# Optimization experiments

Hardware: AMD Instinct MI355X
Metric: run time of the kernel (lower is better)

Reference implementation:

```python
import jax, jax.numpy as jnp
import numpy as np

B, T, K, D, H, HL, S, KN = 4096, 50, 32, 64, 256, 128, 100000, 1000


def setup_inputs() -> dict:
    key = jax.random.key(0)
    ks = jax.random.split(key, 24)
    inp = {
        "uididx": jax.random.randint(ks[0], (B,), 0, S, dtype=jnp.int32),
        "kcodeidx": jax.random.randint(ks[1], (B, K), 0, KN, dtype=jnp.int32),
        "kcode_len": jax.random.randint(ks[2], (B,), 1, K + 1, dtype=jnp.int32),
        "qidemb": jax.random.normal(ks[3], (B, T, D), dtype=jnp.float32),
        "qid_len": jax.random.randint(ks[4], (B,), 1, T + 1, dtype=jnp.int32),
        # embedding tables
        "stuE": jax.random.normal(ks[5], (S, D), dtype=jnp.float32) * 0.1,
        "knE": jax.random.normal(ks[6], (KN, D), dtype=jnp.float32) * 0.1,
        # Theta DNN params
        "T_W1": jax.random.normal(ks[7], (D, H), dtype=jnp.float32) * (1.0 / np.sqrt(D)),
        "T_b1": jnp.zeros((H,), jnp.float32),
        "T_W2": jax.random.normal(ks[8], (H, 1), dtype=jnp.float32) * (1.0 / np.sqrt(H)),
        "T_b2": jnp.zeros((1,), jnp.float32),
        # A DNN params
        "A_W1": jax.random.normal(ks[9], (D, H), dtype=jnp.float32) * (1.0 / np.sqrt(D)),
        "A_b1": jnp.zeros((H,), jnp.float32),
        "A_W2": jax.random.normal(ks[10], (H, 1), dtype=jnp.float32) * (1.0 / np.sqrt(H)),
        "A_b2": jnp.zeros((1,), jnp.float32),
        # LSTM params (gate order i,f,g,o) + output head
        "L_Wi": jax.random.normal(ks[11], (D, 4 * HL), dtype=jnp.float32) * (1.0 / np.sqrt(D)),
        "L_Wh": jax.random.normal(ks[12], (HL, 4 * HL), dtype=jnp.float32) * (1.0 / np.sqrt(HL)),
        "L_b": jnp.zeros((4 * HL,), jnp.float32),
        "L_Wo": jax.random.normal(ks[13], (HL, 1), dtype=jnp.float32) * (1.0 / np.sqrt(HL)),
        "L_bo": jnp.zeros((1,), jnp.float32),
    }
    return inp


def _dnn(x, W1, b1, W2, b2):
    return jnp.tanh(x @ W1 + b1) @ W2 + b2


def _lstm_last(x, lengths, Wi, Wh, b):
    # x: [B,T,D]; returns last valid hidden state [B,HL]
    xg = jnp.einsum('btd,dh->bth', x, Wi) + b  # precomputed input projections
    h0 = jnp.zeros((x.shape[0], Wh.shape[0]), x.dtype)

    def step(carry, inp):
        h, c = carry
        g_x, t = inp
        g = g_x + h @ Wh
        i, f, gg, o = jnp.split(g, 4, axis=-1)
        c2 = jax.nn.sigmoid(f) * c + jax.nn.sigmoid(i) * jnp.tanh(gg)
        h2 = jax.nn.sigmoid(o) * jnp.tanh(c2)
        upd = (t < lengths)[:, None]
        return (jnp.where(upd, h2, h), jnp.where(upd, c2, c)), None

    (h, _), _ = jax.lax.scan(step, (h0, h0), (xg.transpose(1, 0, 2), jnp.arange(x.shape[1])))
    return h


def reference(uididx, kcodeidx, kcode_len, qidemb, qid_len, stuE, knE,
              T_W1, T_b1, T_W2, T_b2, A_W1, A_b1, A_W2, A_b2,
              L_Wi, L_Wh, L_b, L_Wo, L_bo):
    stu = stuE[uididx]            # [B,D]
    kemb = knE[kcodeidx]          # [B,K,D]
    kmask = jnp.arange(kcodeidx.shape[1])[None, :] < kcode_len[:, None]  # [B,K]
    kmf = kmask.astype(kemb.dtype)

    # per-student mastery: sigmoid(kemb @ stu / 5), then masked reductions
    mastery = jax.nn.sigmoid(jnp.einsum('bkd,bd->bk', kemb, stu) / 5.0)
    mastvec = jnp.einsum('bk,bkd->bd', mastery * kmf, kemb)  # sum(mastery * kemb)
    avec = jnp.einsum('bk,bkd->bd', kmf, kemb)               # sum(kemb)

    # scaled dot-product attention: q=qidemb, k=v=kemb, scale=0.15
    scores = jnp.einsum('btd,bkd->btk', qidemb, kemb) * 0.15
    scores = jnp.where(kmask[:, None, :], scores, -1e9)
    attw = jax.nn.softmax(scores, axis=-1)
    bvec = jnp.einsum('btk,bkd->btd', attw, kemb)            # [B,T,D]

    t = _dnn(mastvec, T_W1, T_b1, T_W2, T_b2)                             # theta [B,1]
    a = 8.0 * (jax.nn.sigmoid(jnp.abs(_dnn(avec, A_W1, A_b1, A_W2, A_b2))) - 0.5)
    hT = _lstm_last(bvec, qid_len, L_Wi, L_Wh, L_b)
    b = 8.0 * (jax.nn.sigmoid(hT @ L_Wo + L_bo) - 0.5)                    # [B,1]

    return jax.nn.sigmoid(a * (t - b))  # IRT response probability [B,1]
```

## Files before the change

kernel.cpp:

```cpp
#include <hip/hip_runtime.h>
#include <math.h>

#define B_  4096
#define T_  50
#define K_  32
#define D_  64
#define H_  256
#define HL_ 128
#define G4_ 512

typedef __attribute__((ext_vector_type(8))) short bf16x8;
typedef __attribute__((ext_vector_type(4))) float f32x4;

__device__ __forceinline__ float fast_exp(float x){ return __expf(x); }
__device__ __forceinline__ float fast_rcp(float x){ return __builtin_amdgcn_rcpf(x); }
__device__ __forceinline__ float sigmoidf_(float x){ return fast_rcp(1.f + fast_exp(-x)); }
__device__ __forceinline__ float tanhf_(float x){ return 1.f - 2.f*fast_rcp(1.f + fast_exp(2.f*x)); }

__device__ __forceinline__ short f2bf(float f){
  union { float f; unsigned u; } v; v.f = f;
  unsigned r = v.u + 0x7FFFu + ((v.u >> 16) & 1u);
  return (short)(r >> 16);
}
__device__ __forceinline__ float bf2f(short s){
  union { unsigned u; float f; } v; v.u = ((unsigned)(unsigned short)s) << 16;
  return v.f;
}

__device__ __forceinline__ float wave_reduce_sum(float v){
  #pragma unroll
  for (int off = 32; off; off >>= 1) v += __shfl_xor(v, off);
  return v;
}

#define KROW 72
#define PROW 40

__global__ __launch_bounds__(256) void head_kernel(
    const int* __restrict__ uididx, const int* __restrict__ kcodeidx,
    const int* __restrict__ kcode_len, const float* __restrict__ qidemb,
    const int* __restrict__ qid_len, const float* __restrict__ stuE,
    const float* __restrict__ knE,
    const float* __restrict__ T_W1, const float* __restrict__ T_b1,
    const float* __restrict__ T_W2, const float* __restrict__ T_b2,
    const float* __restrict__ A_W1, const float* __restrict__ A_b1,
    const float* __restrict__ A_W2, const float* __restrict__ A_b2,
    short* __restrict__ bvec, float* __restrict__ t_val, float* __restrict__ a_val)
{
  __shared__ __align__(16) short s_kemb[K_*KROW];
  __shared__ __align__(16) short s_kembT[D_*PROW];
  __shared__ __align__(16) short s_p[64*PROW];
  __shared__ float s_stu[D_];
  __shared__ float s_mast[K_];
  __shared__ float s_kmf[K_];
  __shared__ float s_mvec[D_];
  __shared__ float s_avec[D_];
  __shared__ float s_redT[4];
  __shared__ float s_redA[4];

  const int b    = blockIdx.x;
  const int tid  = threadIdx.x;
  const int lane = tid & 63;
  const int w    = tid >> 6;
  const int l15  = lane & 15;
  const int quad = lane >> 4;
  const int klen = kcode_len[b];
  const int qlen = qid_len[b];

  if (tid < D_) s_stu[tid] = stuE[uididx[b]*D_ + tid];
  #pragma unroll
  for (int i = tid; i < 512; i += 256){
    int k = i >> 4, f4 = i & 15;
    const float4 v = *(const float4*)&knE[(size_t)kcodeidx[b*K_ + k]*D_ + f4*4];
    short4 b4; b4.x = f2bf(v.x); b4.y = f2bf(v.y); b4.z = f2bf(v.z); b4.w = f2bf(v.w);
    *(short4*)&s_kemb[k*KROW + f4*4] = b4;
    int d = f4*4;
    s_kembT[(d+0)*PROW + k] = b4.x;
    s_kembT[(d+1)*PROW + k] = b4.y;
    s_kembT[(d+2)*PROW + k] = b4.z;
    s_kembT[(d+3)*PROW + k] = b4.w;
  }
  __syncthreads();

  {
    int k = tid >> 3, l8 = tid & 7;
    float s = 0.f;
    #pragma unroll
    for (int j = 0; j < 8; ++j){
      int d = l8 + 8*((j + k) & 7);
      s += s_stu[d] * bf2f(s_kemb[k*KROW + d]);
    }
    s += __shfl_xor(s, 1); s += __shfl_xor(s, 2); s += __shfl_xor(s, 4);
    if (l8 == 0){
      float valid = (k < klen) ? 1.f : 0.f;
      s_mast[k] = valid * sigmoidf_(s * 0.2f);
      s_kmf[k]  = valid;
    }
  }
  __syncthreads();

  if (tid < D_){
    float mv = 0.f, av = 0.f;
    #pragma unroll 4
    for (int k = 0; k < K_; ++k){
      float e = bf2f(s_kemb[k*KROW + tid]);
      mv += s_mast[k] * e;
      av += s_kmf[k]  * e;
    }
    s_mvec[tid] = mv; s_avec[tid] = av;
  }
  __syncthreads();

  {
    const int qrow = w*16 + l15;
    bf16x8 aq[2];
    #pragma unroll
    for (int kt = 0; kt < 2; ++kt){
      if (qrow < qlen){
        const float4 v0 = *(const float4*)&qidemb[((size_t)b*T_ + qrow)*D_ + kt*32 + quad*8];
        const float4 v1 = *(const float4*)&qidemb[((size_t)b*T_ + qrow)*D_ + kt*32 + quad*8 + 4];
        aq[kt][0]=f2bf(v0.x); aq[kt][1]=f2bf(v0.y); aq[kt][2]=f2bf(v0.z); aq[kt][3]=f2bf(v0.w);
        aq[kt][4]=f2bf(v1.x); aq[kt][5]=f2bf(v1.y); aq[kt][6]=f2bf(v1.z); aq[kt][7]=f2bf(v1.w);
      } else {
        aq[kt][0]=0; aq[kt][1]=0; aq[kt][2]=0; aq[kt][3]=0;
        aq[kt][4]=0; aq[kt][5]=0; aq[kt][6]=0; aq[kt][7]=0;
      }
    }
    f32x4 zero = {0.f, 0.f, 0.f, 0.f};
    f32x4 accs[2] = {zero, zero};
    #pragma unroll
    for (int kt = 0; kt < 2; ++kt){
      #pragma unroll
      for (int nt = 0; nt < 2; ++nt){
        bf16x8 bk = *(const bf16x8*)&s_kemb[(nt*16 + l15)*KROW + kt*32 + quad*8];
        accs[nt] = __builtin_amdgcn_mfma_f32_16x16x32_bf16(aq[kt], bk, accs[nt], 0, 0, 0);
      }
    }
    #pragma unroll
    for (int r = 0; r < 4; ++r){
      float v0 = (l15      < klen) ? accs[0][r]*0.15f : -1e9f;
      float v1 = (l15 + 16 < klen) ? accs[1][r]*0.15f : -1e9f;
      float mx = fmaxf(v0, v1);
      #pragma unroll
      for (int off = 1; off < 16; off <<= 1) mx = fmaxf(mx, __shfl_xor(mx, off));
      float e0 = fast_exp(v0 - mx), e1 = fast_exp(v1 - mx);
      float sm = e0 + e1;
      #pragma unroll
      for (int off = 1; off < 16; off <<= 1) sm += __shfl_xor(sm, off);
      float inv = fast_rcp(sm);
      int row = w*16 + quad*4 + r;
      s_p[row*PROW + l15]      = f2bf(e0 * inv);
      s_p[row*PROW + 16 + l15] = f2bf(e1 * inv);
    }
    bf16x8 ap = *(const bf16x8*)&s_p[(w*16 + l15)*PROW + quad*8];
    #pragma unroll
    for (int nt = 0; nt < 4; ++nt){
      bf16x8 bv = *(const bf16x8*)&s_kembT[(nt*16 + l15)*PROW + quad*8];
      f32x4 acco = __builtin_amdgcn_mfma_f32_16x16x32_bf16(ap, bv, zero, 0, 0, 0);
      #pragma unroll
      for (int r = 0; r < 4; ++r){
        int t = w*16 + quad*4 + r;
        if (t < qlen) bvec[((size_t)b*T_ + t)*D_ + nt*16 + l15] = f2bf(acco[r]);
      }
    }
  }

  {
    float accT = T_b1[tid];
    float accA = A_b1[tid];
    #pragma unroll 4
    for (int d = 0; d < D_; ++d){
      float mv = s_mvec[d], av = s_avec[d];
      accT += mv * T_W1[d*H_ + tid];
      accA += av * A_W1[d*H_ + tid];
    }
    float termT = tanhf_(accT) * T_W2[tid];
    float termA = tanhf_(accA) * A_W2[tid];
    termT = wave_reduce_sum(termT);
    termA = wave_reduce_sum(termA);
    if (lane == 0){ s_redT[w] = termT; s_redA[w] = termA; }
    __syncthreads();
    if (tid == 0){
      t_val[b] = s_redT[0] + s_redT[1] + s_redT[2] + s_redT[3] + T_b2[0];
      float v = s_redA[0] + s_redA[1] + s_redA[2] + s_redA[3] + A_b2[0];
      a_val[b] = 8.f * (sigmoidf_(fabsf(v)) - 0.5f);
    }
  }
}

#define HROW 280

__global__ __launch_bounds__(512) void lstm_kernel(
    const short* __restrict__ bvec, const int* __restrict__ qid_len,
    const float* __restrict__ L_Wi, const float* __restrict__ L_Wh,
    const float* __restrict__ L_b,  const float* __restrict__ L_Wo,
    const float* __restrict__ L_bo, const float* __restrict__ t_val,
    const float* __restrict__ a_val, float* __restrict__ out)
{
  __shared__ __align__(16) short s_A[16*HROW];
  __shared__ int s_len[16];

  const int tid  = threadIdx.x;
  const int s0   = blockIdx.x * 16;
  const int w    = tid >> 6;
  const int lane = tid & 63;
  const int l15  = lane & 15;
  const int quad = lane >> 4;

  bf16x8 wf[4][6];
  f32x4  biasv4[4];
  #pragma unroll
  for (int g = 0; g < 4; ++g){
    const int col = g*128 + w*16 + l15;
    #pragma unroll
    for (int r = 0; r < 4; ++r) biasv4[g][r] = L_b[g*128 + w*16 + quad*4 + r];
    #pragma unroll
    for (int kt = 0; kt < 6; ++kt){
      #pragma unroll
      for (int j = 0; j < 8; ++j){
        int k = kt*32 + quad*8 + j;
        float v = (k < D_) ? L_Wi[k*G4_ + col] : L_Wh[(k-D_)*G4_ + col];
        wf[g][kt][j] = f2bf(v);
      }
    }
  }

  for (int p = tid; p < 16*HROW; p += 512) s_A[p] = 0;
  if (tid < 16) s_len[tid] = qid_len[s0 + tid];
  __syncthreads();

  int maxlen = 0;
  #pragma unroll
  for (int i = 0; i < 16; ++i) maxlen = max(maxlen, s_len[i]);
  const int mylen = s_len[l15];
  float c_reg[4] = {0.f,0.f,0.f,0.f};
  float h_reg[4] = {0.f,0.f,0.f,0.f};

  const short* gx = bvec + (size_t)(s0 + l15)*T_*D_ + quad*8;
  bf16x8 xA0 = *(const bf16x8*)(gx);
  bf16x8 xA1 = *(const bf16x8*)(gx + 32);
  bf16x8 xB0 = xA0, xB1 = xA1;
  if (1 < maxlen){ xB0 = *(const bf16x8*)(gx + D_); xB1 = *(const bf16x8*)(gx + D_ + 32); }
  __syncthreads();

#define MF(Aop, Bop, Cop) __builtin_amdgcn_mfma_f32_16x16x32_bf16((Aop), (Bop), (Cop), 0, 0, 0)

#define LSTM_STEP(TI, XB, XC0, XC1) do {                                       \
    const int hb_ = (XB) ^ 1;                                                  \
    const bf16x8 ah0 = *(const bf16x8*)&s_A[l15*HROW + hb_*128 +  0 + quad*8]; \
    const bf16x8 ah1 = *(const bf16x8*)&s_A[l15*HROW + hb_*128 + 32 + quad*8]; \
    const bf16x8 ah2 = *(const bf16x8*)&s_A[l15*HROW + hb_*128 + 64 + quad*8]; \
    const bf16x8 ah3 = *(const bf16x8*)&s_A[l15*HROW + hb_*128 + 96 + quad*8]; \
    f32x4 a0_ = biasv4[0], a1_ = biasv4[1], a2_ = biasv4[2], a3_ = biasv4[3];  \
    a0_ = MF(wf[0][0], XC0, a0_); a0_ = MF(wf[0][1], XC1, a0_);                \
    a1_ = MF(wf[1][0], XC0, a1_); a1_ = MF(wf[1][1], XC1, a1_);                \
    a2_ = MF(wf[2][0], XC0, a2_); a2_ = MF(wf[2][1], XC1, a2_);                \
    a3_ = MF(wf[3][0], XC0, a3_); a3_ = MF(wf[3][1], XC1, a3_);                \
    if ((TI) + 2 < maxlen){                                                    \
      XC0 = *(const bf16x8*)(gx + ((TI)+2)*D_);                                \
      XC1 = *(const bf16x8*)(gx + ((TI)+2)*D_ + 32);                           \
    }                                                                          \
    a0_ = MF(wf[0][2], ah0, a0_); a0_ = MF(wf[0][3], ah1, a0_);                \
    a0_ = MF(wf[0][4], ah2, a0_); a0_ = MF(wf[0][5], ah3, a0_);                \
    a1_ = MF(wf[1][2], ah0, a1_); a1_ = MF(wf[1][3], ah1, a1_);                \
    a1_ = MF(wf[1][4], ah2, a1_); a1_ = MF(wf[1][5], ah3, a1_);                \
    float si_[4], sf_[4], tg_[4], so_[4];                                      \
    _Pragma("unroll") for (int r = 0; r < 4; ++r) si_[r] = sigmoidf_(a0_[r]);  \
    a2_ = MF(wf[2][2], ah0, a2_); a2_ = MF(wf[2][3], ah1, a2_);                \
    a2_ = MF(wf[2][4], ah2, a2_); a2_ = MF(wf[2][5], ah3, a2_);                \
    _Pragma("unroll") for (int r = 0; r < 4; ++r) sf_[r] = sigmoidf_(a1_[r]);  \
    a3_ = MF(wf[3][2], ah0, a3_); a3_ = MF(wf[3][3], ah1, a3_);                \
    a3_ = MF(wf[3][4], ah2, a3_); a3_ = MF(wf[3][5], ah3, a3_);                \
    _Pragma("unroll") for (int r = 0; r < 4; ++r) tg_[r] = tanhf_(a2_[r]);     \
    _Pragma("unroll") for (int r = 0; r < 4; ++r) so_[r] = sigmoidf_(a3_[r]);  \
    const bool upd_ = (TI) < mylen;                                            \
    _Pragma("unroll")                                                          \
    for (int r = 0; r < 4; ++r){                                               \
      float c2 = sf_[r]*c_reg[r] + si_[r]*tg_[r];                              \
      float h2 = so_[r]*tanhf_(c2);                                            \
      c_reg[r] = upd_ ? c2 : c_reg[r];                                         \
      h_reg[r] = upd_ ? h2 : h_reg[r];                                         \
    }                                                                          \
    uint2 hp_;                                                                 \
    hp_.x = (unsigned)(unsigned short)f2bf(h_reg[0])                           \
          | ((unsigned)(unsigned short)f2bf(h_reg[1]) << 16);                  \
    hp_.y = (unsigned)(unsigned short)f2bf(h_reg[2])                           \
          | ((unsigned)(unsigned short)f2bf(h_reg[3]) << 16);                  \
    *(uint2*)&s_A[l15*HROW + (XB)*128 + w*16 + quad*4] = hp_;                  \
    __syncthreads();                                                           \
  } while(0)

  int t = 0;
  for (; t + 1 < maxlen; t += 2){
    LSTM_STEP(t,   0, xA0, xA1);
    LSTM_STEP(t+1, 1, xB0, xB1);
  }
  if (t < maxlen) LSTM_STEP(t, 0, xA0, xA1);
#undef LSTM_STEP
#undef MF

  const int xbLast = (maxlen - 1) & 1;
  for (int s2 = w; s2 < 16; s2 += 8){
    float h0 = bf2f(s_A[s2*HROW + xbLast*128 + lane]);
    float h1 = bf2f(s_A[s2*HROW + xbLast*128 + 64 + lane]);
    float part = h0*L_Wo[lane] + h1*L_Wo[64+lane];
    part = wave_reduce_sum(part);
    if (lane == 0){
      float bb = 8.f * (sigmoidf_(part + L_bo[0]) - 0.5f);
      out[s0+s2] = sigmoidf_(a_val[s0+s2] * (t_val[s0+s2] - bb));
    }
  }
}

extern "C" void kernel_launch(void* const* d_in, const int* in_sizes, int n_in,
                              void* d_out, int out_size, void* d_ws, size_t ws_size,
                              hipStream_t stream)
{
  (void)in_sizes; (void)n_in; (void)out_size; (void)ws_size;
  const int*   uididx    = (const int*)  d_in[0];
  const int*   kcodeidx  = (const int*)  d_in[1];
  const int*   kcode_len = (const int*)  d_in[2];
  const float* qidemb    = (const float*)d_in[3];
  const int*   qid_len   = (const int*)  d_in[4];
  const float* stuE      = (const float*)d_in[5];
  const float* knE       = (const float*)d_in[6];
  const float* T_W1      = (const float*)d_in[7];
  const float* T_b1      = (const float*)d_in[8];
  const float* T_W2      = (const float*)d_in[9];
  const float* T_b2      = (const float*)d_in[10];
  const float* A_W1      = (const float*)d_in[11];
  const float* A_b1      = (const float*)d_in[12];
  const float* A_W2      = (const float*)d_in[13];
  const float* A_b2      = (const float*)d_in[14];
  const float* L_Wi      = (const float*)d_in[15];
  const float* L_Wh      = (const float*)d_in[16];
  const float* L_b       = (const float*)d_in[17];
  const float* L_Wo      = (const float*)d_in[18];
  const float* L_bo      = (const float*)d_in[19];
  float* out = (float*)d_out;

  short* bvec  = (short*)d_ws;
  float* t_val = (float*)(bvec + (size_t)B_*T_*D_);
  float* a_val = t_val + B_;

  hipLaunchKernelGGL(head_kernel, dim3(B_), dim3(256), 0, stream,
    uididx, kcodeidx, kcode_len, qidemb, qid_len, stuE, knE,
    T_W1, T_b1, T_W2, T_b2, A_W1, A_b1, A_W2, A_b2,
    bvec, t_val, a_val);

  hipLaunchKernelGGL(lstm_kernel, dim3(B_/16), dim3(512), 0, stream,
    bvec, qid_len, L_Wi, L_Wh, L_b, L_Wo, L_bo, t_val, a_val, out);
}
```

Measured before the change: 219.1 us.

## Split theta/A DNN into separate batched kernel reusing weights across 16 samples

Moves the two small MLPs (theta and A) out of the per-sample head kernel into a new kernel that processes 16 samples per block. Each block loads every W1 weight once and reuses it across 16 samples in registers, instead of every sample re-reading the full 64x256 weight matrices. The intermediate mastery and sum vectors now go through global memory, which adds one extra kernel launch and a small round trip.

```diff
diff --git a/kernel.cpp b/kernel.cpp
--- a/kernel.cpp
+++ b/kernel.cpp
@@ -41,11 +41,7 @@
     const int* __restrict__ kcode_len, const float* __restrict__ qidemb,
     const int* __restrict__ qid_len, const float* __restrict__ stuE,
     const float* __restrict__ knE,
-    const float* __restrict__ T_W1, const float* __restrict__ T_b1,
-    const float* __restrict__ T_W2, const float* __restrict__ T_b2,
-    const float* __restrict__ A_W1, const float* __restrict__ A_b1,
-    const float* __restrict__ A_W2, const float* __restrict__ A_b2,
-    short* __restrict__ bvec, float* __restrict__ t_val, float* __restrict__ a_val)
+    short* __restrict__ bvec, float* __restrict__ mvecG, float* __restrict__ avecG)
 {
   __shared__ __align__(16) short s_kemb[K_*KROW];
   __shared__ __align__(16) short s_kembT[D_*PROW];
@@ -53,10 +49,6 @@
   __shared__ float s_stu[D_];
   __shared__ float s_mast[K_];
   __shared__ float s_kmf[K_];
-  __shared__ float s_mvec[D_];
-  __shared__ float s_avec[D_];
-  __shared__ float s_redT[4];
-  __shared__ float s_redA[4];
 
   const int b    = blockIdx.x;
   const int tid  = threadIdx.x;
@@ -107,7 +99,8 @@
       mv += s_mast[k] * e;
       av += s_kmf[k]  * e;
     }
-    s_mvec[tid] = mv; s_avec[tid] = av;
+    mvecG[(size_t)b*D_ + tid] = mv;
+    avecG[(size_t)b*D_ + tid] = av;
   }
   __syncthreads();
 
@@ -164,27 +157,63 @@
       }
     }
   }
+}
+
+__global__ __launch_bounds__(256) void dnn_kernel(
+    const float* __restrict__ mvecG, const float* __restrict__ avecG,
+    const float* __restrict__ T_W1, const float* __restrict__ T_b1,
+    const float* __restrict__ T_W2, const float* __restrict__ T_b2,
+    const float* __restrict__ A_W1, const float* __restrict__ A_b1,
+    const float* __restrict__ A_W2, const float* __restrict__ A_b2,
+    float* __restrict__ t_val, float* __restrict__ a_val)
+{
+  __shared__ float s_mv[16*D_];
+  __shared__ float s_av[16*D_];
+  __shared__ float s_redT[4][16];
+  __shared__ float s_redA[4][16];
+
+  const int tid  = threadIdx.x;
+  const int s0   = blockIdx.x * 16;
+  const int lane = tid & 63;
+  const int w    = tid >> 6;
 
   {
-    float accT = T_b1[tid];
-    float accA = A_b1[tid];
-    #pragma unroll 4
-    for (int d = 0; d < D_; ++d){
-      float mv = s_mvec[d], av = s_avec[d];
-      accT += mv * T_W1[d*H_ + tid];
-      accA += av * A_W1[d*H_ + tid];
-    }
-    float termT = tanhf_(accT) * T_W2[tid];
-    float termA = tanhf_(accA) * A_W2[tid];
-    termT = wave_reduce_sum(termT);
-    termA = wave_reduce_sum(termA);
-    if (lane == 0){ s_redT[w] = termT; s_redA[w] = termA; }
-    __syncthreads();
-    if (tid == 0){
-      t_val[b] = s_redT[0] + s_redT[1] + s_redT[2] + s_redT[3] + T_b2[0];
-      float v = s_redA[0] + s_redA[1] + s_redA[2] + s_redA[3] + A_b2[0];
-      a_val[b] = 8.f * (sigmoidf_(fabsf(v)) - 0.5f);
-    }
+    const float4* gmv = (const float4*)(mvecG + (size_t)s0*D_);
+    const float4* gav = (const float4*)(avecG + (size_t)s0*D_);
+    ((float4*)s_mv)[tid] = gmv[tid];
+    ((float4*)s_av)[tid] = gav[tid];
+  }
+  __syncthreads();
+
+  const int col = tid;
+  float accT[16], accA[16];
+  {
+    const float bT = T_b1[col], bA = A_b1[col];
+    #pragma unroll
+    for (int s = 0; s < 16; ++s){ accT[s] = bT; accA[s] = bA; }
+  }
+  #pragma unroll 4
+  for (int d = 0; d < D_; ++d){
+    const float wT = T_W1[d*H_ + col];
+    const float wA = A_W1[d*H_ + col];
+    #pragma unroll
+    for (int s = 0; s < 16; ++s){
+      accT[s] += s_mv[s*D_ + d] * wT;
+      accA[s] += s_av[s*D_ + d] * wA;
+    }
+  }
+  const float w2T = T_W2[col], w2A = A_W2[col];
+  #pragma unroll
+  for (int s = 0; s < 16; ++s){
+    float tT = wave_reduce_sum(tanhf_(accT[s]) * w2T);
+    float tA = wave_reduce_sum(tanhf_(accA[s]) * w2A);
+    if (lane == 0){ s_redT[w][s] = tT; s_redA[w][s] = tA; }
+  }
+  __syncthreads();
+  if (tid < 16){
+    t_val[s0+tid] = s_redT[0][tid] + s_redT[1][tid] + s_redT[2][tid] + s_redT[3][tid] + T_b2[0];
+    float v = s_redA[0][tid] + s_redA[1][tid] + s_redA[2][tid] + s_redA[3][tid] + A_b2[0];
+    a_val[s0+tid] = 8.f * (sigmoidf_(fabsf(v)) - 0.5f);
   }
 }
 
@@ -340,13 +369,18 @@
   float* out = (float*)d_out;
 
   short* bvec  = (short*)d_ws;
-  float* t_val = (float*)(bvec + (size_t)B_*T_*D_);
+  float* mvecG = (float*)(bvec + (size_t)B_*T_*D_);
+  float* avecG = mvecG + (size_t)B_*D_;
+  float* t_val = avecG + (size_t)B_*D_;
   float* a_val = t_val + B_;
 
   hipLaunchKernelGGL(head_kernel, dim3(B_), dim3(256), 0, stream,
     uididx, kcodeidx, kcode_len, qidemb, qid_len, stuE, knE,
-    T_W1, T_b1, T_W2, T_b2, A_W1, A_b1, A_W2, A_b2,
-    bvec, t_val, a_val);
+    bvec, mvecG, avecG);
+
+  hipLaunchKernelGGL(dnn_kernel, dim3(B_/16), dim3(256), 0, stream,
+    mvecG, avecG, T_W1, T_b1, T_W2, T_b2, A_W1, A_b1, A_W2, A_b2,
+    t_val, a_val);
 
   hipLaunchKernelGGL(lstm_kernel, dim3(B_/16), dim3(512), 0, stream,
     bvec, qid_len, L_Wi, L_Wh, L_b, L_Wo, L_bo, t_val, a_val, out);
```

Measured after the change: 231.1 us. 5.4% more time.

## Split LSTM gate computation across two wave groups with LDS exchange

Applied to the files above, without the earlier changes.

Doubles the LSTM block to 1024 threads. One group of waves computes the i/f gates and the other computes the g/o gates. Each step the partial gate results are swapped through shared memory so each half can finish two of the four hidden elements. The aim is to halve the serial MFMA chain per wave on the recurrent critical path, at the cost of an extra barrier and LDS traffic per timestep and more waves per block.

```diff
diff --git a/kernel.cpp b/kernel.cpp
--- a/kernel.cpp
+++ b/kernel.cpp
@@ -190,7 +190,7 @@
 
 #define HROW 280
 
-__global__ __launch_bounds__(512) void lstm_kernel(
+__global__ __launch_bounds__(1024) void lstm_kernel(
     const short* __restrict__ bvec, const int* __restrict__ qid_len,
     const float* __restrict__ L_Wi, const float* __restrict__ L_Wh,
     const float* __restrict__ L_b,  const float* __restrict__ L_Wo,
@@ -198,34 +198,39 @@
     const float* __restrict__ a_val, float* __restrict__ out)
 {
   __shared__ __align__(16) short s_A[16*HROW];
+  __shared__ __align__(16) float s_eIF[16][130][2];
+  __shared__ __align__(16) float s_eGO[16][130][2];
   __shared__ int s_len[16];
 
-  const int tid  = threadIdx.x;
-  const int s0   = blockIdx.x * 16;
-  const int w    = tid >> 6;
-  const int lane = tid & 63;
-  const int l15  = lane & 15;
-  const int quad = lane >> 4;
-
-  bf16x8 wf[4][6];
-  f32x4  biasv4[4];
+  const int tid   = threadIdx.x;
+  const int s0    = blockIdx.x * 16;
+  const int w     = tid >> 6;
+  const int lane  = tid & 63;
+  const int l15   = lane & 15;
+  const int quad  = lane >> 4;
+  const int ghalf = w >> 3;
+  const int wsub  = w & 7;
+
+  bf16x8 wf[2][6];
+  f32x4  biasv4[2];
   #pragma unroll
-  for (int g = 0; g < 4; ++g){
-    const int col = g*128 + w*16 + l15;
-    #pragma unroll
-    for (int r = 0; r < 4; ++r) biasv4[g][r] = L_b[g*128 + w*16 + quad*4 + r];
+  for (int gg = 0; gg < 2; ++gg){
+    const int gate = ghalf*2 + gg;
+    const int col  = gate*128 + wsub*16 + l15;
+    #pragma unroll
+    for (int r = 0; r < 4; ++r) biasv4[gg][r] = L_b[gate*128 + wsub*16 + quad*4 + r];
     #pragma unroll
     for (int kt = 0; kt < 6; ++kt){
       #pragma unroll
       for (int j = 0; j < 8; ++j){
         int k = kt*32 + quad*8 + j;
         float v = (k < D_) ? L_Wi[k*G4_ + col] : L_Wh[(k-D_)*G4_ + col];
-        wf[g][kt][j] = f2bf(v);
+        wf[gg][kt][j] = f2bf(v);
       }
     }
   }
 
-  for (int p = tid; p < 16*HROW; p += 512) s_A[p] = 0;
+  for (int p = tid; p < 16*HROW; p += 1024) s_A[p] = 0;
   if (tid < 16) s_len[tid] = qid_len[s0 + tid];
   __syncthreads();
 
@@ -233,15 +238,14 @@
   #pragma unroll
   for (int i = 0; i < 16; ++i) maxlen = max(maxlen, s_len[i]);
   const int mylen = s_len[l15];
-  float c_reg[4] = {0.f,0.f,0.f,0.f};
-  float h_reg[4] = {0.f,0.f,0.f,0.f};
+  float c_reg[2] = {0.f, 0.f};
+  float h_reg[2] = {0.f, 0.f};
 
   const short* gx = bvec + (size_t)(s0 + l15)*T_*D_ + quad*8;
   bf16x8 xA0 = *(const bf16x8*)(gx);
   bf16x8 xA1 = *(const bf16x8*)(gx + 32);
   bf16x8 xB0 = xA0, xB1 = xA1;
   if (1 < maxlen){ xB0 = *(const bf16x8*)(gx + D_); xB1 = *(const bf16x8*)(gx + D_ + 32); }
-  __syncthreads();
 
 #define MF(Aop, Bop, Cop) __builtin_amdgcn_mfma_f32_16x16x32_bf16((Aop), (Bop), (Cop), 0, 0, 0)
 
@@ -251,42 +255,56 @@
     const bf16x8 ah1 = *(const bf16x8*)&s_A[l15*HROW + hb_*128 + 32 + quad*8]; \
     const bf16x8 ah2 = *(const bf16x8*)&s_A[l15*HROW + hb_*128 + 64 + quad*8]; \
     const bf16x8 ah3 = *(const bf16x8*)&s_A[l15*HROW + hb_*128 + 96 + quad*8]; \
-    f32x4 a0_ = biasv4[0], a1_ = biasv4[1], a2_ = biasv4[2], a3_ = biasv4[3];  \
-    a0_ = MF(wf[0][0], XC0, a0_); a0_ = MF(wf[0][1], XC1, a0_);                \
-    a1_ = MF(wf[1][0], XC0, a1_); a1_ = MF(wf[1][1], XC1, a1_);                \
-    a2_ = MF(wf[2][0], XC0, a2_); a2_ = MF(wf[2][1], XC1, a2_);                \
-    a3_ = MF(wf[3][0], XC0, a3_); a3_ = MF(wf[3][1], XC1, a3_);                \
+    f32x4 a0_ = biasv4[0], a1_ = biasv4[1];                                    \
+    a0_ = MF(wf[0][0], XC0, a0_); a1_ = MF(wf[1][0], XC0, a1_);                \
+    a0_ = MF(wf[0][1], XC1, a0_); a1_ = MF(wf[1][1], XC1, a1_);                \
     if ((TI) + 2 < maxlen){                                                    \
       XC0 = *(const bf16x8*)(gx + ((TI)+2)*D_);                                \
       XC1 = *(const bf16x8*)(gx + ((TI)+2)*D_ + 32);                           \
     }                                                                          \
-    a0_ = MF(wf[0][2], ah0, a0_); a0_ = MF(wf[0][3], ah1, a0_);                \
-    a0_ = MF(wf[0][4], ah2, a0_); a0_ = MF(wf[0][5], ah3, a0_);                \
-    a1_ = MF(wf[1][2], ah0, a1_); a1_ = MF(wf[1][3], ah1, a1_);                \
-    a1_ = MF(wf[1][4], ah2, a1_); a1_ = MF(wf[1][5], ah3, a1_);                \
-    float si_[4], sf_[4], tg_[4], so_[4];                                      \
-    _Pragma("unroll") for (int r = 0; r < 4; ++r) si_[r] = sigmoidf_(a0_[r]);  \
-    a2_ = MF(wf[2][2], ah0, a2_); a2_ = MF(wf[2][3], ah1, a2_);                \
-    a2_ = MF(wf[2][4], ah2, a2_); a2_ = MF(wf[2][5], ah3, a2_);                \
-    _Pragma("unroll") for (int r = 0; r < 4; ++r) sf_[r] = sigmoidf_(a1_[r]);  \
-    a3_ = MF(wf[3][2], ah0, a3_); a3_ = MF(wf[3][3], ah1, a3_);                \
-    a3_ = MF(wf[3][4], ah2, a3_); a3_ = MF(wf[3][5], ah3, a3_);                \
-    _Pragma("unroll") for (int r = 0; r < 4; ++r) tg_[r] = tanhf_(a2_[r]);     \
-    _Pragma("unroll") for (int r = 0; r < 4; ++r) so_[r] = sigmoidf_(a3_[r]);  \
+    a0_ = MF(wf[0][2], ah0, a0_); a1_ = MF(wf[1][2], ah0, a1_);                \
+    a0_ = MF(wf[0][3], ah1, a0_); a1_ = MF(wf[1][3], ah1, a1_);                \
+    a0_ = MF(wf[0][4], ah2, a0_); a1_ = MF(wf[1][4], ah2, a1_);                \
+    a0_ = MF(wf[0][5], ah3, a0_); a1_ = MF(wf[1][5], ah3, a1_);                \
+                     \
+    if (ghalf == 0){                                                           \
+      float4 snd; snd.x = a0_[2]; snd.y = a1_[2]; snd.z = a0_[3]; snd.w = a1_[3]; \
+      *(float4*)&s_eIF[l15][wsub*16 + quad*4 + 2][0] = snd;                    \
+    } else {                                                                   \
+      float4 snd; snd.x = a0_[0]; snd.y = a1_[0]; snd.z = a0_[1]; snd.w = a1_[1]; \
+      *(float4*)&s_eGO[l15][wsub*16 + quad*4][0] = snd;                        \
+    }                                                                          \
+    __syncthreads();                                                           \
     const bool upd_ = (TI) < mylen;                                            \
-    _Pragma("unroll")                                                          \
-    for (int r = 0; r < 4; ++r){                                               \
-      float c2 = sf_[r]*c_reg[r] + si_[r]*tg_[r];                              \
-      float h2 = so_[r]*tanhf_(c2);                                            \
-      c_reg[r] = upd_ ? c2 : c_reg[r];                                         \
-      h_reg[r] = upd_ ? h2 : h_reg[r];                                         \
+    if (ghalf == 0){                                                           \
+      const float4 rcv = *(const float4*)&s_eGO[l15][wsub*16 + quad*4][0];     \
+      _Pragma("unroll")                                                        \
+      for (int k = 0; k < 2; ++k){                                             \
+        float gi = a0_[k], gf = a1_[k];                                        \
+        float gg_ = (k ? rcv.z : rcv.x), go = (k ? rcv.w : rcv.y);             \
+        float c2 = sigmoidf_(gf)*c_reg[k] + sigmoidf_(gi)*tanhf_(gg_);         \
+        float h2 = sigmoidf_(go)*tanhf_(c2);                                   \
+        c_reg[k] = upd_ ? c2 : c_reg[k];                                       \
+        h_reg[k] = upd_ ? h2 : h_reg[k];                                       \
+      }                                                                        \
+      unsigned hp_ = (unsigned)(unsigned short)f2bf(h_reg[0])                  \
+                   | ((unsigned)(unsigned short)f2bf(h_reg[1]) << 16);         \
+      *(unsigned*)&s_A[l15*HROW + (XB)*128 + wsub*16 + quad*4] = hp_;          \
+    } else {                                                                   \
+      const float4 rcv = *(const float4*)&s_eIF[l15][wsub*16 + quad*4 + 2][0]; \
+      _Pragma("unroll")                                                        \
+      for (int k = 0; k < 2; ++k){                                             \
+        float gi = (k ? rcv.z : rcv.x), gf = (k ? rcv.w : rcv.y);              \
+        float gg_ = a0_[2+k], go = a1_[2+k];                                   \
+        float c2 = sigmoidf_(gf)*c_reg[k] + sigmoidf_(gi)*tanhf_(gg_);         \
+        float h2 = sigmoidf_(go)*tanhf_(c2);                                   \
+        c_reg[k] = upd_ ? c2 : c_reg[k];                                       \
+        h_reg[k] = upd_ ? h2 : h_reg[k];                                       \
+      }                                                                        \
+      unsigned hp_ = (unsigned)(unsigned short)f2bf(h_reg[0])                  \
+                   | ((unsigned)(unsigned short)f2bf(h_reg[1]) << 16);         \
+      *(unsigned*)&s_A[l15*HROW + (XB)*128 + wsub*16 + quad*4 + 2] = hp_;      \
     }                                                                          \
-    uint2 hp_;                                                                 \
-    hp_.x = (unsigned)(unsigned short)f2bf(h_reg[0])                           \
-          | ((unsigned)(unsigned short)f2bf(h_reg[1]) << 16);                  \
-    hp_.y = (unsigned)(unsigned short)f2bf(h_reg[2])                           \
-          | ((unsigned)(unsigned short)f2bf(h_reg[3]) << 16);                  \
-    *(uint2*)&s_A[l15*HROW + (XB)*128 + w*16 + quad*4] = hp_;                  \
     __syncthreads();                                                           \
   } while(0)
 
@@ -300,7 +318,8 @@
 #undef MF
 
   const int xbLast = (maxlen - 1) & 1;
-  for (int s2 = w; s2 < 16; s2 += 8){
+  {
+    const int s2 = w;
     float h0 = bf2f(s_A[s2*HROW + xbLast*128 + lane]);
     float h1 = bf2f(s_A[s2*HROW + xbLast*128 + 64 + lane]);
     float part = h0*L_Wo[lane] + h1*L_Wo[64+lane];
@@ -348,6 +367,6 @@
     T_W1, T_b1, T_W2, T_b2, A_W1, A_b1, A_W2, A_b2,
     bvec, t_val, a_val);
 
-  hipLaunchKernelGGL(lstm_kernel, dim3(B_/16), dim3(512), 0, stream,
+  hipLaunchKernelGGL(lstm_kernel, dim3(B_/16), dim3(1024), 0, stream,
     bvec, qid_len, L_Wi, L_Wh, L_b, L_Wo, L_bo, t_val, a_val, out);
 }
```

Measured after the change: 240.7 us. 1.1x slower.
